# Kernel tuning notes

Hardware: AMD Instinct MI355X
Metric: run time of the kernel (lower is better)

The kernel has to match this reference:

```python
import jax, jax.numpy as jnp
import numpy as np

N = 100000   # nodes
E = 1600000  # edges
D = 128      # in_dim
H = 128      # hidden_dim
C = 40       # num_classes
EPS = 1e-5   # LayerNorm eps (torch default)


def setup_inputs() -> dict:
    key = jax.random.key(0)
    ks = jax.random.split(key, 16)
    x = jax.random.normal(ks[0], (N, D), dtype=jnp.float32)
    edge_index = jax.random.randint(ks[1], (2, E), 0, N, dtype=jnp.int64)
    s = 1.0 / np.sqrt(D)
    inp = {"x": x, "edge_index": edge_index}
    # 3 GCN layers: weight [in, H], bias [H]; LayerNorm gamma/beta [H]
    for i in range(3):
        inp[f"W{i}"] = jax.random.normal(ks[2 + i], (D if i == 0 else H, H), dtype=jnp.float32) * s
        inp[f"b{i}"] = jnp.zeros((H,), jnp.float32)
        inp[f"g{i}"] = jnp.ones((H,), jnp.float32)
        inp[f"be{i}"] = jnp.zeros((H,), jnp.float32)
    inp["Wc"] = jax.random.normal(ks[10], (H, C), dtype=jnp.float32) * (1.0 / np.sqrt(H))
    inp["bc"] = jnp.zeros((C,), jnp.float32)
    return inp


def _layer_norm(h, g, b):
    mu = jnp.mean(h, axis=-1, keepdims=True)
    var = jnp.var(h, axis=-1, keepdims=True)  # biased, matches torch
    return (h - mu) * jax.lax.rsqrt(var + EPS) * g + b


def _gcn_conv(x, W, b, src, dst, enorm, dinv2):
    # GCNConv: D^{-1/2}(A+I)D^{-1/2} X W + b (self-loops handled analytically)
    h = x @ W                                   # [N, H]
    agg = jax.ops.segment_sum(h[src] * enorm[:, None], dst, num_segments=N)
    return agg + h * dinv2[:, None] + b


def reference(x, edge_index, W0, b0, g0, be0, W1, b1, g1, be1, W2, b2, g2, be2, Wc, bc):
    src, dst = edge_index[0], edge_index[1]
    # degree with self-loops (GCNConv adds self-loops by default)
    deg = jnp.zeros((N,), x.dtype).at[dst].add(1.0) + 1.0
    dinv = jax.lax.rsqrt(deg)
    enorm = dinv[src] * dinv[dst]               # per-edge normalization
    dinv2 = dinv * dinv                         # self-loop normalization

    Ws, bs, gs, bes = (W0, W1, W2), (b0, b1, b2), (g0, g1, g2), (be0, be1, be2)
    for i in range(3):
        x_in = x
        x = _gcn_conv(x, Ws[i], bs[i], src, dst, enorm, dinv2)
        x = _layer_norm(x, gs[i], bes[i])
        x = jax.nn.elu(x)
        if i > 0:
            x = x + x_in
        # dropout: eval mode / p=0 -> identity
    return x @ Wc + bc
```

## Files before the change

kernel.cpp:

```cpp
#include <hip/hip_runtime.h>
#include <math.h>

#define N_NODES 100000
#define N_EDGES 1600000
#define DIM     128
#define NCLS    40
#define NBUCK   196
#define P1_CH   4096
#define P1_GRID 391

typedef _Float16 f16x8 __attribute__((ext_vector_type(8)));
typedef _Float16 f16x2 __attribute__((ext_vector_type(2)));
typedef float    f32x4 __attribute__((ext_vector_type(4)));

__device__ inline unsigned short f16bits(float f) {
    union { _Float16 h; unsigned short u; } cv;
    cv.h = (_Float16)f;
    return cv.u;
}
__device__ inline f16x2 as_h2(unsigned u) {
    union { unsigned u; f16x2 h; } cv;
    cv.u = u;
    return cv.h;
}
__device__ inline unsigned as_u(f16x2 h) {
    union { f16x2 h; unsigned u; } cv;
    cv.h = h;
    return cv.u;
}
__device__ inline unsigned pack_h2(float lo, float hi) {
    f16x2 h;
    h.x = (_Float16)lo;
    h.y = (_Float16)hi;
    return as_u(h);
}
__device__ inline int wave_incl_scan(int v, int lane) {
#pragma unroll
    for (int off = 1; off < 64; off <<= 1) {
        int x = __shfl_up(v, off, 64);
        if (lane >= off) v += x;
    }
    return v;
}

__global__ __launch_bounds__(256) void setup_misc(const float* __restrict__ W0,
                                                  const float* __restrict__ W1,
                                                  const float* __restrict__ W2,
                                                  const float* __restrict__ Wc,
                                                  const int* __restrict__ ei,
                                                  unsigned short* __restrict__ Wsw0,
                                                  unsigned short* __restrict__ Wsw1,
                                                  unsigned short* __restrict__ Wsw2,
                                                  unsigned short* __restrict__ Wcsw,
                                                  int* __restrict__ bcnt) {
    int blk = blockIdx.x;
    if (blk < 192) {
        const float* W = (blk < 64) ? W0 : (blk < 128) ? W1 : W2;
        unsigned short* Wsw = (blk < 64) ? Wsw0 : (blk < 128) ? Wsw1 : Wsw2;
        int o = (blk & 63) * 256 + threadIdx.x;
        int f = o >> 9;
        int l = (o >> 3) & 63;
        int j = o & 7;
        int n = f >> 2;
        int s = f & 3;
        int k = s * 32 + (l >> 4) * 8 + j;
        int c = (l & 15) * 8 + n;
        Wsw[o] = f16bits(W[k * DIM + c]);
    } else if (blk < 216) {
        int o = (blk - 192) * 256 + threadIdx.x;
        int f = o >> 9;
        int l = (o >> 3) & 63;
        int j = o & 7;
        int n = f >> 2;
        int s = f & 3;
        int k = s * 32 + (l >> 4) * 8 + j;
        int c = (l & 15) * 3 + n;
        Wcsw[o] = (c < NCLS) ? f16bits(Wc[k * NCLS + c]) : (unsigned short)0;
    } else {
        __shared__ int h[256];
        const int t  = threadIdx.x;
        const int e0 = (blk - 216) * P1_CH;
        const int cnt = min(P1_CH, N_EDGES - e0);
        h[t] = 0;
        __syncthreads();
        for (int i = t; i < cnt; i += 256)
            atomicAdd(&h[ei[N_EDGES + e0 + i] >> 9], 1);
        __syncthreads();
        if (h[t]) atomicAdd(&bcnt[t], h[t]);
    }
}

__global__ __launch_bounds__(256) void bscan(const int* __restrict__ bcnt,
                                             int* __restrict__ bbase,
                                             int* __restrict__ bcur) {
    __shared__ int wtot[4];
    int t = threadIdx.x;
    int lane = t & 63, wv = t >> 6;
    int v = (t < NBUCK) ? bcnt[t] : 0;
    int incl = wave_incl_scan(v, lane);
    if (lane == 63) wtot[wv] = incl;
    __syncthreads();
    int prefix = 0;
    for (int i = 0; i < wv; ++i) prefix += wtot[i];
    incl += prefix;
    int excl = incl - v;
    if (t < NBUCK) {
        bbase[t] = excl;
        bcur[t]  = excl;
    }
    if (t == 0) bbase[NBUCK] = N_EDGES;
}

__global__ __launch_bounds__(256) void bucket_p1(const int* __restrict__ ei,
                                                 int* __restrict__ bcur,
                                                 unsigned* __restrict__ tmp) {
    __shared__ int  hist[256];
    __shared__ int  lscan[256];
    __shared__ int  rank[256];
    __shared__ int  gbase[256];
    __shared__ int  wtot[4];
    __shared__ int2 stage[P1_CH];
    const int t  = threadIdx.x;
    const int lane = t & 63, wv = t >> 6;
    const int e0 = blockIdx.x * P1_CH;
    const int cnt = min(P1_CH, N_EDGES - e0);

    hist[t] = 0;
    __syncthreads();

    int2 ed[16];
#pragma unroll
    for (int i = 0; i < 16; ++i) {
        int idx = t + i * 256;
        if (idx < cnt) {
            int s = ei[e0 + idx];
            int d = ei[N_EDGES + e0 + idx];
            ed[i] = make_int2(s, d);
            atomicAdd(&hist[d >> 9], 1);
        }
    }
    __syncthreads();

    int hv = hist[t];
    int incl = wave_incl_scan(hv, lane);
    if (lane == 63) wtot[wv] = incl;
    __syncthreads();
    int prefix = 0;
    for (int i = 0; i < wv; ++i) prefix += wtot[i];
    incl += prefix;
    int excl = incl - hv;
    lscan[t] = excl;
    rank[t]  = excl;
    if (hv > 0) gbase[t] = atomicAdd(&bcur[t], hv);
    __syncthreads();

#pragma unroll
    for (int i = 0; i < 16; ++i) {
        int idx = t + i * 256;
        if (idx < cnt) {
            int b = ed[i].y >> 9;
            int p = atomicAdd(&rank[b], 1);
            stage[p] = ed[i];
        }
    }
    __syncthreads();

    for (int p = t; p < cnt; p += 256) {
        int2 v = stage[p];
        int b = v.y >> 9;
        tmp[gbase[b] + (p - lscan[b])] = ((unsigned)v.x << 9) | ((unsigned)v.y & 511u);
    }
}

__global__ __launch_bounds__(256) void bucket_p2(const unsigned* __restrict__ tmp,
                                                 const int* __restrict__ bbase,
                                                 int* __restrict__ rowptr,
                                                 float* __restrict__ dinv,
                                                 unsigned* __restrict__ rec) {
    __shared__ int cnt[512];
    __shared__ int cur[512];
    __shared__ int wtot[4];
    const int t  = threadIdx.x;
    const int lane = t & 63, wv = t >> 6;
    const int b  = blockIdx.x;
    const int d0 = b << 9;
    const int dend = min(d0 + 512, N_NODES);
    const int nn = dend - d0;

    cnt[t] = 0;
    cnt[t + 256] = 0;
    __syncthreads();

    const int beg = bbase[b];
    const int end = bbase[b + 1];
    for (int idx = beg + t; idx < end; idx += 256)
        atomicAdd(&cnt[tmp[idx] & 511u], 1);
    __syncthreads();

    int c0 = cnt[2 * t];
    int c1 = cnt[2 * t + 1];
    int pv = c0 + c1;
    int incl = wave_incl_scan(pv, lane);
    if (lane == 63) wtot[wv] = incl;
    __syncthreads();
    int prefix = 0;
    for (int i = 0; i < wv; ++i) prefix += wtot[i];
    incl += prefix;
    int excl = incl - pv;
    int base0 = beg + excl;
    int base1 = base0 + c0;
    cur[2 * t]     = base0;
    cur[2 * t + 1] = base1;
    if (2 * t < nn) {
        rowptr[d0 + 2 * t] = base0;
        dinv[d0 + 2 * t]   = rsqrtf((float)c0 + 1.0f);
    }
    if (2 * t + 1 < nn) {
        rowptr[d0 + 2 * t + 1] = base1;
        dinv[d0 + 2 * t + 1]   = rsqrtf((float)c1 + 1.0f);
    }
    if (b == NBUCK - 1 && t == 0) rowptr[N_NODES] = N_EDGES;
    __syncthreads();

    for (int idx = beg + t; idx < end; idx += 256) {
        unsigned u = tmp[idx];
        int pos = atomicAdd(&cur[u & 511u], 1);
        rec[pos] = (u >> 9) << 8;
    }
}

__global__ __launch_bounds__(256) void gemm_mfma_f(const float* __restrict__ X,
                                                   const unsigned short* __restrict__ Wsw,
                                                   const float* __restrict__ dinv,
                                                   unsigned short* __restrict__ H) {
    __shared__ unsigned short wlds[32 * 512];
    const int tid   = threadIdx.x;
    const int lane  = tid & 63;
    const int wave  = tid >> 6;
    const int row0w = blockIdx.x * 64 + wave * 16;
    const int m = lane & 15;
    const int q = lane >> 4;

    {
        const uint4* srcp = (const uint4*)Wsw;
        uint4*       dstp = (uint4*)wlds;
#pragma unroll
        for (int i = 0; i < 8; ++i) dstp[tid + i * 256] = srcp[tid + i * 256];
    }
    __syncthreads();

    int r = row0w + m;
    if (r >= N_NODES) r = N_NODES - 1;
    const float* xp = X + (size_t)r * DIM + q * 8;
    f16x8 af[4];
#pragma unroll
    for (int s = 0; s < 4; ++s) {
        float4 x0 = *(const float4*)(xp + s * 32);
        float4 x1 = *(const float4*)(xp + s * 32 + 4);
        f16x8 v;
        v[0] = (_Float16)x0.x; v[1] = (_Float16)x0.y;
        v[2] = (_Float16)x0.z; v[3] = (_Float16)x0.w;
        v[4] = (_Float16)x1.x; v[5] = (_Float16)x1.y;
        v[6] = (_Float16)x1.z; v[7] = (_Float16)x1.w;
        af[s] = v;
    }

    f32x4 acc[8];
    f32x4 z = {0.f, 0.f, 0.f, 0.f};
#pragma unroll
    for (int n = 0; n < 8; ++n) acc[n] = z;

    const unsigned short* wl = wlds + lane * 8;
#pragma unroll
    for (int s = 0; s < 4; ++s)
#pragma unroll
        for (int n = 0; n < 8; ++n) {
            f16x8 wf = *(const f16x8*)(wl + ((n * 4 + s) << 9));
            acc[n] = __builtin_amdgcn_mfma_f32_16x16x32_f16(af[s], wf, acc[n], 0, 0, 0);
        }

#pragma unroll
    for (int j = 0; j < 4; ++j) {
        int row = row0w + q * 4 + j;
        if (row < N_NODES) {
            float dv = dinv[row];
            uint4 o;
            o.x = pack_h2(acc[0][j] * dv, acc[1][j] * dv);
            o.y = pack_h2(acc[2][j] * dv, acc[3][j] * dv);
            o.z = pack_h2(acc[4][j] * dv, acc[5][j] * dv);
            o.w = pack_h2(acc[6][j] * dv, acc[7][j] * dv);
            *(uint4*)(H + (size_t)row * DIM + m * 8) = o;
        } else {
            uint4 zz = make_uint4(0u, 0u, 0u, 0u);
            *(uint4*)(H + (size_t)row * DIM + m * 8) = zz;
        }
    }
}

__global__ __launch_bounds__(256) void gemm_mfma_h(const unsigned short* __restrict__ Xh,
                                                   const unsigned short* __restrict__ Wsw,
                                                   const float* __restrict__ dinv,
                                                   unsigned short* __restrict__ H) {
    __shared__ unsigned short wlds[32 * 512];
    const int tid   = threadIdx.x;
    const int lane  = tid & 63;
    const int wave  = tid >> 6;
    const int row0w = blockIdx.x * 64 + wave * 16;
    const int m = lane & 15;
    const int q = lane >> 4;

    {
        const uint4* srcp = (const uint4*)Wsw;
        uint4*       dstp = (uint4*)wlds;
#pragma unroll
        for (int i = 0; i < 8; ++i) dstp[tid + i * 256] = srcp[tid + i * 256];
    }
    __syncthreads();

    int r = row0w + m;
    if (r >= N_NODES) r = N_NODES - 1;
    const unsigned short* xp = Xh + (size_t)r * DIM + q * 8;
    f16x8 af[4];
#pragma unroll
    for (int s = 0; s < 4; ++s) af[s] = *(const f16x8*)(xp + s * 32);

    f32x4 acc[8];
    f32x4 z = {0.f, 0.f, 0.f, 0.f};
#pragma unroll
    for (int n = 0; n < 8; ++n) acc[n] = z;

    const unsigned short* wl = wlds + lane * 8;
#pragma unroll
    for (int s = 0; s < 4; ++s)
#pragma unroll
        for (int n = 0; n < 8; ++n) {
            f16x8 wf = *(const f16x8*)(wl + ((n * 4 + s) << 9));
            acc[n] = __builtin_amdgcn_mfma_f32_16x16x32_f16(af[s], wf, acc[n], 0, 0, 0);
        }

#pragma unroll
    for (int j = 0; j < 4; ++j) {
        int row = row0w + q * 4 + j;
        if (row < N_NODES) {
            float dv = dinv[row];
            uint4 o;
            o.x = pack_h2(acc[0][j] * dv, acc[1][j] * dv);
            o.y = pack_h2(acc[2][j] * dv, acc[3][j] * dv);
            o.z = pack_h2(acc[4][j] * dv, acc[5][j] * dv);
            o.w = pack_h2(acc[6][j] * dv, acc[7][j] * dv);
            *(uint4*)(H + (size_t)row * DIM + m * 8) = o;
        } else {
            uint4 zz = make_uint4(0u, 0u, 0u, 0u);
            *(uint4*)(H + (size_t)row * DIM + m * 8) = zz;
        }
    }
}

__global__ __launch_bounds__(256) void agg_ln(const unsigned short* __restrict__ Hh,
                                              const unsigned short* __restrict__ xin,
                                              const float* __restrict__ dinv,
                                              const float* __restrict__ bias,
                                              const float* __restrict__ g,
                                              const float* __restrict__ be,
                                              const int* __restrict__ rowptr,
                                              const unsigned* __restrict__ rec,
                                              unsigned short* __restrict__ outb) {
    const int tid  = threadIdx.x;
    const int lane = tid & 63;
    const int l16  = tid & 15;
    const int gb   = lane & 48;
    const int node = blockIdx.x * 16 + (tid >> 4);
    const int beg  = rowptr[node];
    const int end  = rowptr[node + 1];
    const char* Hb8 = (const char*)Hh;
    const unsigned laneoff = (unsigned)l16 * 16;
    const unsigned sentin  = (unsigned)N_NODES << 8;

    f16x2 accA[4], accB[4], accC[4], accD[4];
    f16x2 hz = {(_Float16)0.f, (_Float16)0.f};
#pragma unroll
    for (int k = 0; k < 4; ++k) { accA[k] = hz; accB[k] = hz; accC[k] = hz; accD[k] = hz; }

    for (int e0 = beg; e0 < end; e0 += 16) {
        int cnt = min(end - e0, 16);
        unsigned sv = (l16 < cnt) ? rec[e0 + l16] : sentin;
        int cntR = (cnt + 7) & ~7;
        for (int j = 0; j < cntR; j += 8) {
            unsigned o0 = (unsigned)__shfl((int)sv, gb + j + 0, 64) + laneoff;
            unsigned o1 = (unsigned)__shfl((int)sv, gb + j + 1, 64) + laneoff;
            unsigned o2 = (unsigned)__shfl((int)sv, gb + j + 2, 64) + laneoff;
            unsigned o3 = (unsigned)__shfl((int)sv, gb + j + 3, 64) + laneoff;
            unsigned o4 = (unsigned)__shfl((int)sv, gb + j + 4, 64) + laneoff;
            unsigned o5 = (unsigned)__shfl((int)sv, gb + j + 5, 64) + laneoff;
            unsigned o6 = (unsigned)__shfl((int)sv, gb + j + 6, 64) + laneoff;
            unsigned o7 = (unsigned)__shfl((int)sv, gb + j + 7, 64) + laneoff;
            uint4 u0 = *(const uint4*)(Hb8 + o0);
            uint4 u1 = *(const uint4*)(Hb8 + o1);
            uint4 u2 = *(const uint4*)(Hb8 + o2);
            uint4 u3 = *(const uint4*)(Hb8 + o3);
            uint4 u4 = *(const uint4*)(Hb8 + o4);
            uint4 u5 = *(const uint4*)(Hb8 + o5);
            uint4 u6 = *(const uint4*)(Hb8 + o6);
            uint4 u7 = *(const uint4*)(Hb8 + o7);
            accA[0] += as_h2(u0.x); accA[1] += as_h2(u0.y); accA[2] += as_h2(u0.z); accA[3] += as_h2(u0.w);
            accB[0] += as_h2(u1.x); accB[1] += as_h2(u1.y); accB[2] += as_h2(u1.z); accB[3] += as_h2(u1.w);
            accC[0] += as_h2(u2.x); accC[1] += as_h2(u2.y); accC[2] += as_h2(u2.z); accC[3] += as_h2(u2.w);
            accD[0] += as_h2(u3.x); accD[1] += as_h2(u3.y); accD[2] += as_h2(u3.z); accD[3] += as_h2(u3.w);
            accA[0] += as_h2(u4.x); accA[1] += as_h2(u4.y); accA[2] += as_h2(u4.z); accA[3] += as_h2(u4.w);
            accB[0] += as_h2(u5.x); accB[1] += as_h2(u5.y); accB[2] += as_h2(u5.z); accB[3] += as_h2(u5.w);
            accC[0] += as_h2(u6.x); accC[1] += as_h2(u6.y); accC[2] += as_h2(u6.z); accC[3] += as_h2(u6.w);
            accD[0] += as_h2(u7.x); accD[1] += as_h2(u7.y); accD[2] += as_h2(u7.z); accD[3] += as_h2(u7.w);
        }
    }

#pragma unroll
    for (int k = 0; k < 4; ++k) accA[k] = (accA[k] + accB[k]) + (accC[k] + accD[k]);

    const float dv = dinv[node];
    const unsigned nodeoff = ((unsigned)node << 8) + laneoff;
    uint4 hv = *(const uint4*)(Hb8 + nodeoff);
    const int c0 = l16 * 8;
    float4 bb0 = *(const float4*)(bias + c0);
    float4 bb1 = *(const float4*)(bias + c0 + 4);
    f16x2 h0 = as_h2(hv.x), h1 = as_h2(hv.y), h2 = as_h2(hv.z), h3 = as_h2(hv.w);

    float a[8];
    a[0] = ((float)accA[0].x + (float)h0.x) * dv + bb0.x;
    a[1] = ((float)accA[0].y + (float)h0.y) * dv + bb0.y;
    a[2] = ((float)accA[1].x + (float)h1.x) * dv + bb0.z;
    a[3] = ((float)accA[1].y + (float)h1.y) * dv + bb0.w;
    a[4] = ((float)accA[2].x + (float)h2.x) * dv + bb1.x;
    a[5] = ((float)accA[2].y + (float)h2.y) * dv + bb1.y;
    a[6] = ((float)accA[3].x + (float)h3.x) * dv + bb1.z;
    a[7] = ((float)accA[3].y + (float)h3.y) * dv + bb1.w;

    float s1 = 0.f, s2 = 0.f;
#pragma unroll
    for (int i = 0; i < 8; ++i) { s1 += a[i]; s2 += a[i] * a[i]; }
#pragma unroll
    for (int mk = 1; mk <= 8; mk <<= 1) {
        s1 += __shfl_xor(s1, mk, 64);
        s2 += __shfl_xor(s2, mk, 64);
    }
    float mean = s1 * (1.0f / 128.0f);
    float var  = s2 * (1.0f / 128.0f) - mean * mean;
    float rr   = rsqrtf(var + 1e-5f);

    float4 gg0 = *(const float4*)(g + c0);
    float4 gg1 = *(const float4*)(g + c0 + 4);
    float4 ee0 = *(const float4*)(be + c0);
    float4 ee1 = *(const float4*)(be + c0 + 4);

    float r[8];
    r[0] = (a[0] - mean) * rr * gg0.x + ee0.x;
    r[1] = (a[1] - mean) * rr * gg0.y + ee0.y;
    r[2] = (a[2] - mean) * rr * gg0.z + ee0.z;
    r[3] = (a[3] - mean) * rr * gg0.w + ee0.w;
    r[4] = (a[4] - mean) * rr * gg1.x + ee1.x;
    r[5] = (a[5] - mean) * rr * gg1.y + ee1.y;
    r[6] = (a[6] - mean) * rr * gg1.z + ee1.z;
    r[7] = (a[7] - mean) * rr * gg1.w + ee1.w;
#pragma unroll
    for (int i = 0; i < 8; ++i) r[i] = r[i] > 0.0f ? r[i] : expm1f(r[i]);

    if (xin) {
        uint4 xv = *(const uint4*)((const char*)xin + nodeoff);
        f16x2 x0 = as_h2(xv.x), x1 = as_h2(xv.y), x2 = as_h2(xv.z), x3 = as_h2(xv.w);
        r[0] += (float)x0.x; r[1] += (float)x0.y;
        r[2] += (float)x1.x; r[3] += (float)x1.y;
        r[4] += (float)x2.x; r[5] += (float)x2.y;
        r[6] += (float)x3.x; r[7] += (float)x3.y;
    }

    uint4 o;
    o.x = pack_h2(r[0], r[1]);
    o.y = pack_h2(r[2], r[3]);
    o.z = pack_h2(r[4], r[5]);
    o.w = pack_h2(r[6], r[7]);
    *(uint4*)((char*)outb + nodeoff) = o;
}

__global__ __launch_bounds__(256) void classifier_mfma(const unsigned short* __restrict__ Xh,
                                                       const unsigned short* __restrict__ Wcsw,
                                                       const float* __restrict__ bc,
                                                       float* __restrict__ out) {
    __shared__ unsigned short wlds[12 * 512];
    const int tid   = threadIdx.x;
    const int lane  = tid & 63;
    const int wave  = tid >> 6;
    const int row0w = blockIdx.x * 128 + wave * 32;
    const int m = lane & 15;
    const int q = lane >> 4;

    {
        const uint4* srcp = (const uint4*)Wcsw;
        uint4*       dstp = (uint4*)wlds;
#pragma unroll
        for (int i = 0; i < 3; ++i) dstp[tid + i * 256] = srcp[tid + i * 256];
    }
    __syncthreads();

    f16x8 wf[12];
#pragma unroll
    for (int f = 0; f < 12; ++f)
        wf[f] = *(const f16x8*)(wlds + (f << 9) + lane * 8);

    f16x8 af[2][4];
#pragma unroll
    for (int ggr = 0; ggr < 2; ++ggr) {
        int r = row0w + ggr * 16 + m;
        if (r >= N_NODES) r = N_NODES - 1;
        const unsigned short* xp = Xh + (size_t)r * DIM + q * 8;
#pragma unroll
        for (int s = 0; s < 4; ++s) af[ggr][s] = *(const f16x8*)(xp + s * 32);
    }

    f32x4 acc[2][3];
    f32x4 z = {0.f, 0.f, 0.f, 0.f};
#pragma unroll
    for (int ggr = 0; ggr < 2; ++ggr)
#pragma unroll
        for (int n = 0; n < 3; ++n) acc[ggr][n] = z;

#pragma unroll
    for (int s = 0; s < 4; ++s)
#pragma unroll
        for (int n = 0; n < 3; ++n) {
            acc[0][n] = __builtin_amdgcn_mfma_f32_16x16x32_f16(af[0][s], wf[n * 4 + s], acc[0][n], 0, 0, 0);
            acc[1][n] = __builtin_amdgcn_mfma_f32_16x16x32_f16(af[1][s], wf[n * 4 + s], acc[1][n], 0, 0, 0);
        }

    float bcv[3];
#pragma unroll
    for (int n = 0; n < 3; ++n) {
        int c = 3 * m + n;
        bcv[n] = (c < NCLS) ? bc[c] : 0.f;
    }

#pragma unroll
    for (int ggr = 0; ggr < 2; ++ggr)
#pragma unroll
        for (int j = 0; j < 4; ++j) {
            int row = row0w + ggr * 16 + q * 4 + j;
            if (row < N_NODES) {
#pragma unroll
                for (int n = 0; n < 3; ++n) {
                    int c = 3 * m + n;
                    if (c < NCLS)
                        out[(size_t)row * NCLS + c] = acc[ggr][n][j] + bcv[n];
                }
            }
        }
}

extern "C" void kernel_launch(void* const* d_in, const int* in_sizes, int n_in,
                              void* d_out, int out_size, void* d_ws, size_t ws_size,
                              hipStream_t stream) {
    const float* x  = (const float*)d_in[0];
    const int*   ei = (const int*)d_in[1];
    const float* W[3]  = {(const float*)d_in[2], (const float*)d_in[6], (const float*)d_in[10]};
    const float* b[3]  = {(const float*)d_in[3], (const float*)d_in[7], (const float*)d_in[11]};
    const float* g[3]  = {(const float*)d_in[4], (const float*)d_in[8], (const float*)d_in[12]};
    const float* be[3] = {(const float*)d_in[5], (const float*)d_in[9], (const float*)d_in[13]};
    const float* Wc = (const float*)d_in[14];
    const float* bc = (const float*)d_in[15];
    float* out = (float*)d_out;

    char* ws = (char*)d_ws;
    const size_t NP = 400128;
    float* dinv   = (float*)(ws);
    int*   rowptr = (int*)  (ws + NP);
    int*   bcnt   = (int*)  (ws + 2 * NP);
    int*   bbase  = (int*)  (ws + 2 * NP + 1024);
    int*   bcur   = (int*)  (ws + 2 * NP + 2048);
    unsigned* rec = (unsigned*)(ws + 2 * NP + 4096);
    unsigned short* Hh = (unsigned short*)(ws + 2 * NP + 4096 + (size_t)N_EDGES * 8);
    unsigned short* Ah = Hh + (size_t)(N_NODES + 64) * DIM;
    unsigned short* Ch = Ah + (size_t)N_NODES * DIM;
    unsigned short* Wsw0 = Ch + (size_t)N_NODES * DIM;
    unsigned short* Wsw1 = Wsw0 + DIM * DIM;
    unsigned short* Wsw2 = Wsw1 + DIM * DIM;
    unsigned short* Wcsw = Wsw2 + DIM * DIM;
    unsigned* tmp = (unsigned*)Ch;

    hipMemsetAsync(bcnt, 0, 1024, stream);
    setup_misc<<<216 + P1_GRID, 256, 0, stream>>>(W[0], W[1], W[2], Wc, ei,
                                                  Wsw0, Wsw1, Wsw2, Wcsw, bcnt);

    bscan<<<1, 256, 0, stream>>>(bcnt, bbase, bcur);
    bucket_p1<<<P1_GRID, 256, 0, stream>>>(ei, bcur, tmp);
    bucket_p2<<<NBUCK, 256, 0, stream>>>(tmp, bbase, rowptr, dinv, rec);

    const int gemm_grid = (N_NODES + 63) / 64;
    const int cls_grid  = (N_NODES + 127) / 128;
    const int agg_grid  = N_NODES / 16;

    gemm_mfma_f<<<gemm_grid, 256, 0, stream>>>(x, Wsw0, dinv, Hh);
    agg_ln<<<agg_grid, 256, 0, stream>>>(Hh, nullptr, dinv, b[0], g[0], be[0], rowptr, rec, Ch);

    gemm_mfma_h<<<gemm_grid, 256, 0, stream>>>(Ch, Wsw1, dinv, Hh);
    agg_ln<<<agg_grid, 256, 0, stream>>>(Hh, Ch, dinv, b[1], g[1], be[1], rowptr, rec, Ah);

    gemm_mfma_h<<<gemm_grid, 256, 0, stream>>>(Ah, Wsw2, dinv, Hh);
    agg_ln<<<agg_grid, 256, 0, stream>>>(Hh, Ah, dinv, b[2], g[2], be[2], rowptr, rec, Ch);

    classifier_mfma<<<cls_grid, 256, 0, stream>>>(Ch, Wcsw, bc, out);
}
```

Before: 401.5 us.

## Fuse classifier into last aggregation kernel and fold bucket scan into bucketing kernels

The final aggregate+LayerNorm kernel now also computes the classifier. It stages its 16 output rows in LDS and runs the MFMA classifier from there, so the last-layer activations are never written to and reread from global memory. The separate bucket-scan kernel is dropped: each bucket_p1 and bucket_p2 block redoes the small prefix scan over bucket counts, and global offsets come from a zeroed atomic counter. This removes two launches and one full activation round trip, at the cost of redundant per-block scans and only one wave doing MFMA work in each fused block.

```diff
diff --git a/kernel.cpp b/kernel.cpp
--- a/kernel.cpp
+++ b/kernel.cpp
@@ -90,40 +90,23 @@
     }
 }
 
-__global__ __launch_bounds__(256) void bscan(const int* __restrict__ bcnt,
-                                             int* __restrict__ bbase,
-                                             int* __restrict__ bcur) {
-    __shared__ int wtot[4];
-    int t = threadIdx.x;
-    int lane = t & 63, wv = t >> 6;
-    int v = (t < NBUCK) ? bcnt[t] : 0;
-    int incl = wave_incl_scan(v, lane);
-    if (lane == 63) wtot[wv] = incl;
-    __syncthreads();
-    int prefix = 0;
-    for (int i = 0; i < wv; ++i) prefix += wtot[i];
-    incl += prefix;
-    int excl = incl - v;
-    if (t < NBUCK) {
-        bbase[t] = excl;
-        bcur[t]  = excl;
-    }
-    if (t == 0) bbase[NBUCK] = N_EDGES;
-}
-
 __global__ __launch_bounds__(256) void bucket_p1(const int* __restrict__ ei,
-                                                 int* __restrict__ bcur,
+                                                 const int* __restrict__ bcnt,
+                                                 int* __restrict__ boff,
                                                  unsigned* __restrict__ tmp) {
     __shared__ int  hist[256];
     __shared__ int  lscan[256];
     __shared__ int  rank[256];
     __shared__ int  gbase[256];
-    __shared__ int  wtot[4];
+    __shared__ int  wtotA[4];
+    __shared__ int  wtotB[4];
     __shared__ int2 stage[P1_CH];
     const int t  = threadIdx.x;
     const int lane = t & 63, wv = t >> 6;
     const int e0 = blockIdx.x * P1_CH;
     const int cnt = min(P1_CH, N_EDGES - e0);
+
+    int bcv = (t < NBUCK) ? bcnt[t] : 0;
 
     hist[t] = 0;
     __syncthreads();
@@ -142,16 +125,24 @@
     __syncthreads();
 
     int hv = hist[t];
-    int incl = wave_incl_scan(hv, lane);
-    if (lane == 63) wtot[wv] = incl;
-    __syncthreads();
-    int prefix = 0;
-    for (int i = 0; i < wv; ++i) prefix += wtot[i];
-    incl += prefix;
-    int excl = incl - hv;
-    lscan[t] = excl;
-    rank[t]  = excl;
-    if (hv > 0) gbase[t] = atomicAdd(&bcur[t], hv);
+    int inclA = hv, inclB = bcv;
+#pragma unroll
+    for (int off = 1; off < 64; off <<= 1) {
+        int xa = __shfl_up(inclA, off, 64);
+        int xb = __shfl_up(inclB, off, 64);
+        if (lane >= off) { inclA += xa; inclB += xb; }
+    }
+    if (lane == 63) { wtotA[wv] = inclA; wtotB[wv] = inclB; }
+    __syncthreads();
+    int pA = 0, pB = 0;
+    for (int i = 0; i < wv; ++i) { pA += wtotA[i]; pB += wtotB[i]; }
+    inclA += pA;
+    inclB += pB;
+    int exclA = inclA - hv;
+    int exclB = inclB - bcv;
+    lscan[t] = exclA;
+    rank[t]  = exclA;
+    if (hv > 0) gbase[t] = exclB + atomicAdd(&boff[t], hv);
     __syncthreads();
 
 #pragma unroll
@@ -173,13 +164,14 @@
 }
 
 __global__ __launch_bounds__(256) void bucket_p2(const unsigned* __restrict__ tmp,
-                                                 const int* __restrict__ bbase,
+                                                 const int* __restrict__ bcnt,
                                                  int* __restrict__ rowptr,
                                                  float* __restrict__ dinv,
                                                  unsigned* __restrict__ rec) {
     __shared__ int cnt[512];
     __shared__ int cur[512];
     __shared__ int wtot[4];
+    __shared__ int sbeg, send;
     const int t  = threadIdx.x;
     const int lane = t & 63, wv = t >> 6;
     const int b  = blockIdx.x;
@@ -187,12 +179,22 @@
     const int dend = min(d0 + 512, N_NODES);
     const int nn = dend - d0;
 
+    int bcv = (t < NBUCK) ? bcnt[t] : 0;
+    int binc = wave_incl_scan(bcv, lane);
+    if (lane == 63) wtot[wv] = binc;
     cnt[t] = 0;
     cnt[t + 256] = 0;
     __syncthreads();
-
-    const int beg = bbase[b];
-    const int end = bbase[b + 1];
+    {
+        int pfx = 0;
+        for (int i = 0; i < wv; ++i) pfx += wtot[i];
+        binc += pfx;
+        if (t == b) { sbeg = binc - bcv; send = binc; }
+    }
+    __syncthreads();
+
+    const int beg = sbeg;
+    const int end = send;
     for (int idx = beg + t; idx < end; idx += 256)
         atomicAdd(&cnt[tmp[idx] & 511u], 1);
     __syncthreads();
@@ -480,77 +482,171 @@
     *(uint4*)((char*)outb + nodeoff) = o;
 }
 
-__global__ __launch_bounds__(256) void classifier_mfma(const unsigned short* __restrict__ Xh,
-                                                       const unsigned short* __restrict__ Wcsw,
-                                                       const float* __restrict__ bc,
-                                                       float* __restrict__ out) {
-    __shared__ unsigned short wlds[12 * 512];
-    const int tid   = threadIdx.x;
-    const int lane  = tid & 63;
-    const int wave  = tid >> 6;
-    const int row0w = blockIdx.x * 128 + wave * 32;
-    const int m = lane & 15;
-    const int q = lane >> 4;
-
-    {
-        const uint4* srcp = (const uint4*)Wcsw;
-        uint4*       dstp = (uint4*)wlds;
-#pragma unroll
-        for (int i = 0; i < 3; ++i) dstp[tid + i * 256] = srcp[tid + i * 256];
-    }
-    __syncthreads();
-
-    f16x8 wf[12];
-#pragma unroll
-    for (int f = 0; f < 12; ++f)
-        wf[f] = *(const f16x8*)(wlds + (f << 9) + lane * 8);
-
-    f16x8 af[2][4];
-#pragma unroll
-    for (int ggr = 0; ggr < 2; ++ggr) {
-        int r = row0w + ggr * 16 + m;
-        if (r >= N_NODES) r = N_NODES - 1;
-        const unsigned short* xp = Xh + (size_t)r * DIM + q * 8;
-#pragma unroll
-        for (int s = 0; s < 4; ++s) af[ggr][s] = *(const f16x8*)(xp + s * 32);
-    }
-
-    f32x4 acc[2][3];
-    f32x4 z = {0.f, 0.f, 0.f, 0.f};
-#pragma unroll
-    for (int ggr = 0; ggr < 2; ++ggr)
-#pragma unroll
-        for (int n = 0; n < 3; ++n) acc[ggr][n] = z;
-
-#pragma unroll
-    for (int s = 0; s < 4; ++s)
-#pragma unroll
-        for (int n = 0; n < 3; ++n) {
-            acc[0][n] = __builtin_amdgcn_mfma_f32_16x16x32_f16(af[0][s], wf[n * 4 + s], acc[0][n], 0, 0, 0);
-            acc[1][n] = __builtin_amdgcn_mfma_f32_16x16x32_f16(af[1][s], wf[n * 4 + s], acc[1][n], 0, 0, 0);
-        }
-
-    float bcv[3];
-#pragma unroll
-    for (int n = 0; n < 3; ++n) {
-        int c = 3 * m + n;
-        bcv[n] = (c < NCLS) ? bc[c] : 0.f;
-    }
-
-#pragma unroll
-    for (int ggr = 0; ggr < 2; ++ggr)
+__global__ __launch_bounds__(256) void agg_ln_cls(const unsigned short* __restrict__ Hh,
+                                                  const unsigned short* __restrict__ xin,
+                                                  const float* __restrict__ dinv,
+                                                  const float* __restrict__ bias,
+                                                  const float* __restrict__ g,
+                                                  const float* __restrict__ be,
+                                                  const int* __restrict__ rowptr,
+                                                  const unsigned* __restrict__ rec,
+                                                  const unsigned short* __restrict__ Wcsw,
+                                                  const float* __restrict__ bc,
+                                                  float* __restrict__ out) {
+    __shared__ _Float16 hl[16][136];
+    const int tid  = threadIdx.x;
+    const int lane = tid & 63;
+    const int l16  = tid & 15;
+    const int gb   = lane & 48;
+    const int grp  = tid >> 4;
+    const int node0 = blockIdx.x * 16;
+    const int node = node0 + grp;
+    const int beg  = rowptr[node];
+    const int end  = rowptr[node + 1];
+    const char* Hb8 = (const char*)Hh;
+    const unsigned laneoff = (unsigned)l16 * 16;
+    const unsigned sentin  = (unsigned)N_NODES << 8;
+
+    f16x2 accA[4], accB[4], accC[4], accD[4];
+    f16x2 hz = {(_Float16)0.f, (_Float16)0.f};
+#pragma unroll
+    for (int k = 0; k < 4; ++k) { accA[k] = hz; accB[k] = hz; accC[k] = hz; accD[k] = hz; }
+
+    for (int e0 = beg; e0 < end; e0 += 16) {
+        int cnt = min(end - e0, 16);
+        unsigned sv = (l16 < cnt) ? rec[e0 + l16] : sentin;
+        int cntR = (cnt + 7) & ~7;
+        for (int j = 0; j < cntR; j += 8) {
+            unsigned o0 = (unsigned)__shfl((int)sv, gb + j + 0, 64) + laneoff;
+            unsigned o1 = (unsigned)__shfl((int)sv, gb + j + 1, 64) + laneoff;
+            unsigned o2 = (unsigned)__shfl((int)sv, gb + j + 2, 64) + laneoff;
+            unsigned o3 = (unsigned)__shfl((int)sv, gb + j + 3, 64) + laneoff;
+            unsigned o4 = (unsigned)__shfl((int)sv, gb + j + 4, 64) + laneoff;
+            unsigned o5 = (unsigned)__shfl((int)sv, gb + j + 5, 64) + laneoff;
+            unsigned o6 = (unsigned)__shfl((int)sv, gb + j + 6, 64) + laneoff;
+            unsigned o7 = (unsigned)__shfl((int)sv, gb + j + 7, 64) + laneoff;
+            uint4 u0 = *(const uint4*)(Hb8 + o0);
+            uint4 u1 = *(const uint4*)(Hb8 + o1);
+            uint4 u2 = *(const uint4*)(Hb8 + o2);
+            uint4 u3 = *(const uint4*)(Hb8 + o3);
+            uint4 u4 = *(const uint4*)(Hb8 + o4);
+            uint4 u5 = *(const uint4*)(Hb8 + o5);
+            uint4 u6 = *(const uint4*)(Hb8 + o6);
+            uint4 u7 = *(const uint4*)(Hb8 + o7);
+            accA[0] += as_h2(u0.x); accA[1] += as_h2(u0.y); accA[2] += as_h2(u0.z); accA[3] += as_h2(u0.w);
+            accB[0] += as_h2(u1.x); accB[1] += as_h2(u1.y); accB[2] += as_h2(u1.z); accB[3] += as_h2(u1.w);
+            accC[0] += as_h2(u2.x); accC[1] += as_h2(u2.y); accC[2] += as_h2(u2.z); accC[3] += as_h2(u2.w);
+            accD[0] += as_h2(u3.x); accD[1] += as_h2(u3.y); accD[2] += as_h2(u3.z); accD[3] += as_h2(u3.w);
+            accA[0] += as_h2(u4.x); accA[1] += as_h2(u4.y); accA[2] += as_h2(u4.z); accA[3] += as_h2(u4.w);
+            accB[0] += as_h2(u5.x); accB[1] += as_h2(u5.y); accB[2] += as_h2(u5.z); accB[3] += as_h2(u5.w);
+            accC[0] += as_h2(u6.x); accC[1] += as_h2(u6.y); accC[2] += as_h2(u6.z); accC[3] += as_h2(u6.w);
+            accD[0] += as_h2(u7.x); accD[1] += as_h2(u7.y); accD[2] += as_h2(u7.z); accD[3] += as_h2(u7.w);
+        }
+    }
+
+#pragma unroll
+    for (int k = 0; k < 4; ++k) accA[k] = (accA[k] + accB[k]) + (accC[k] + accD[k]);
+
+    const float dv = dinv[node];
+    const unsigned nodeoff = ((unsigned)node << 8) + laneoff;
+    uint4 hv = *(const uint4*)(Hb8 + nodeoff);
+    const int c0 = l16 * 8;
+    float4 bb0 = *(const float4*)(bias + c0);
+    float4 bb1 = *(const float4*)(bias + c0 + 4);
+    f16x2 h0 = as_h2(hv.x), h1 = as_h2(hv.y), h2 = as_h2(hv.z), h3 = as_h2(hv.w);
+
+    float a[8];
+    a[0] = ((float)accA[0].x + (float)h0.x) * dv + bb0.x;
+    a[1] = ((float)accA[0].y + (float)h0.y) * dv + bb0.y;
+    a[2] = ((float)accA[1].x + (float)h1.x) * dv + bb0.z;
+    a[3] = ((float)accA[1].y + (float)h1.y) * dv + bb0.w;
+    a[4] = ((float)accA[2].x + (float)h2.x) * dv + bb1.x;
+    a[5] = ((float)accA[2].y + (float)h2.y) * dv + bb1.y;
+    a[6] = ((float)accA[3].x + (float)h3.x) * dv + bb1.z;
+    a[7] = ((float)accA[3].y + (float)h3.y) * dv + bb1.w;
+
+    float s1 = 0.f, s2 = 0.f;
+#pragma unroll
+    for (int i = 0; i < 8; ++i) { s1 += a[i]; s2 += a[i] * a[i]; }
+#pragma unroll
+    for (int mk = 1; mk <= 8; mk <<= 1) {
+        s1 += __shfl_xor(s1, mk, 64);
+        s2 += __shfl_xor(s2, mk, 64);
+    }
+    float mean = s1 * (1.0f / 128.0f);
+    float var  = s2 * (1.0f / 128.0f) - mean * mean;
+    float rr   = rsqrtf(var + 1e-5f);
+
+    float4 gg0 = *(const float4*)(g + c0);
+    float4 gg1 = *(const float4*)(g + c0 + 4);
+    float4 ee0 = *(const float4*)(be + c0);
+    float4 ee1 = *(const float4*)(be + c0 + 4);
+
+    float r[8];
+    r[0] = (a[0] - mean) * rr * gg0.x + ee0.x;
+    r[1] = (a[1] - mean) * rr * gg0.y + ee0.y;
+    r[2] = (a[2] - mean) * rr * gg0.z + ee0.z;
+    r[3] = (a[3] - mean) * rr * gg0.w + ee0.w;
+    r[4] = (a[4] - mean) * rr * gg1.x + ee1.x;
+    r[5] = (a[5] - mean) * rr * gg1.y + ee1.y;
+    r[6] = (a[6] - mean) * rr * gg1.z + ee1.z;
+    r[7] = (a[7] - mean) * rr * gg1.w + ee1.w;
+#pragma unroll
+    for (int i = 0; i < 8; ++i) r[i] = r[i] > 0.0f ? r[i] : expm1f(r[i]);
+
+    if (xin) {
+        uint4 xv = *(const uint4*)((const char*)xin + nodeoff);
+        f16x2 x0 = as_h2(xv.x), x1 = as_h2(xv.y), x2 = as_h2(xv.z), x3 = as_h2(xv.w);
+        r[0] += (float)x0.x; r[1] += (float)x0.y;
+        r[2] += (float)x1.x; r[3] += (float)x1.y;
+        r[4] += (float)x2.x; r[5] += (float)x2.y;
+        r[6] += (float)x3.x; r[7] += (float)x3.y;
+    }
+
+    uint4 o;
+    o.x = pack_h2(r[0], r[1]);
+    o.y = pack_h2(r[2], r[3]);
+    o.z = pack_h2(r[4], r[5]);
+    o.w = pack_h2(r[6], r[7]);
+    *(uint4*)&hl[grp][l16 * 8] = o;
+    __syncthreads();
+
+    if (tid < 64) {
+        const int m = lane & 15;
+        const int q = lane >> 4;
+
+        f16x8 wf[12];
+#pragma unroll
+        for (int f = 0; f < 12; ++f)
+            wf[f] = *(const f16x8*)(Wcsw + (f << 9) + lane * 8);
+
+        f16x8 af[4];
+#pragma unroll
+        for (int s = 0; s < 4; ++s)
+            af[s] = *(const f16x8*)&hl[m][q * 8 + s * 32];
+
+        f32x4 acc[3];
+        f32x4 z = {0.f, 0.f, 0.f, 0.f};
+#pragma unroll
+        for (int n = 0; n < 3; ++n) acc[n] = z;
+
+#pragma unroll
+        for (int s = 0; s < 4; ++s)
+#pragma unroll
+            for (int n = 0; n < 3; ++n)
+                acc[n] = __builtin_amdgcn_mfma_f32_16x16x32_f16(af[s], wf[n * 4 + s], acc[n], 0, 0, 0);
+
 #pragma unroll
         for (int j = 0; j < 4; ++j) {
-            int row = row0w + ggr * 16 + q * 4 + j;
-            if (row < N_NODES) {
-#pragma unroll
-                for (int n = 0; n < 3; ++n) {
-                    int c = 3 * m + n;
-                    if (c < NCLS)
-                        out[(size_t)row * NCLS + c] = acc[ggr][n][j] + bcv[n];
-                }
+            int row = node0 + q * 4 + j;
+#pragma unroll
+            for (int n = 0; n < 3; ++n) {
+                int c = 3 * m + n;
+                if (c < NCLS)
+                    out[(size_t)row * NCLS + c] = acc[n][j] + bc[c];
             }
         }
+    }
 }
 
 extern "C" void kernel_launch(void* const* d_in, const int* in_sizes, int n_in,
@@ -571,8 +667,7 @@
     float* dinv   = (float*)(ws);
     int*   rowptr = (int*)  (ws + NP);
     int*   bcnt   = (int*)  (ws + 2 * NP);
-    int*   bbase  = (int*)  (ws + 2 * NP + 1024);
-    int*   bcur   = (int*)  (ws + 2 * NP + 2048);
+    int*   boff   = (int*)  (ws + 2 * NP + 1024);
     unsigned* rec = (unsigned*)(ws + 2 * NP + 4096);
     unsigned short* Hh = (unsigned short*)(ws + 2 * NP + 4096 + (size_t)N_EDGES * 8);
     unsigned short* Ah = Hh + (size_t)(N_NODES + 64) * DIM;
@@ -583,16 +678,14 @@
     unsigned short* Wcsw = Wsw2 + DIM * DIM;
     unsigned* tmp = (unsigned*)Ch;
 
-    hipMemsetAsync(bcnt, 0, 1024, stream);
+    hipMemsetAsync(bcnt, 0, 2048, stream);
     setup_misc<<<216 + P1_GRID, 256, 0, stream>>>(W[0], W[1], W[2], Wc, ei,
                                                   Wsw0, Wsw1, Wsw2, Wcsw, bcnt);
 
-    bscan<<<1, 256, 0, stream>>>(bcnt, bbase, bcur);
-    bucket_p1<<<P1_GRID, 256, 0, stream>>>(ei, bcur, tmp);
-    bucket_p2<<<NBUCK, 256, 0, stream>>>(tmp, bbase, rowptr, dinv, rec);
+    bucket_p1<<<P1_GRID, 256, 0, stream>>>(ei, bcnt, boff, tmp);
+    bucket_p2<<<NBUCK, 256, 0, stream>>>(tmp, bcnt, rowptr, dinv, rec);
 
     const int gemm_grid = (N_NODES + 63) / 64;
-    const int cls_grid  = (N_NODES + 127) / 128;
     const int agg_grid  = N_NODES / 16;
 
     gemm_mfma_f<<<gemm_grid, 256, 0, stream>>>(x, Wsw0, dinv, Hh);
@@ -602,7 +695,6 @@
     agg_ln<<<agg_grid, 256, 0, stream>>>(Hh, Ch, dinv, b[1], g[1], be[1], rowptr, rec, Ah);
 
     gemm_mfma_h<<<gemm_grid, 256, 0, stream>>>(Ah, Wsw2, dinv, Hh);
-    agg_ln<<<agg_grid, 256, 0, stream>>>(Hh, Ah, dinv, b[2], g[2], be[2], rowptr, rec, Ch);
-
-    classifier_mfma<<<cls_grid, 256, 0, stream>>>(Ch, Wcsw, bc, out);
-}
+    agg_ln_cls<<<agg_grid, 256, 0, stream>>>(Hh, Ah, dinv, b[2], g[2], be[2], rowptr, rec,
+                                             Wcsw, bc, out);
+}
```

After: 389.4 us. 3.0% less time.
